# Kernel optimization log

Hardware: AMD Instinct MI355X
Metric: run time of the kernel (lower is better)

The kernel has to match this reference:

```python
import jax, jax.numpy as jnp
import numpy as np

B, N, OBS, ACT, H = 262144, 3, 30, 5, 64
IN = OBS + ACT  # 35
NEG_SLOPE_ATT = 0.2   # PyG GATConv default
NEG_SLOPE_MLP = 0.01
LN_EPS = 1e-5


def setup_inputs() -> dict:
    key = jax.random.key(0)
    ks = jax.random.split(key, 24)
    p = lambda k, shape, s=0.1: jax.random.normal(k, shape, jnp.float32) * s
    return {
        "obs": jax.random.normal(ks[0], (B, N * OBS), jnp.float32),
        "action": jax.random.normal(ks[1], (B, N * ACT), jnp.float32),
        "adj_matrix": jax.random.randint(ks[2], (B, N, N), 0, 2, jnp.int32),
        # GAT layer 1 (in=35 -> out=64, 1 head)
        "W1": p(ks[3], (IN, H)), "a1s": p(ks[4], (H,)), "a1d": p(ks[5], (H,)), "b1": jnp.zeros((H,), jnp.float32),
        # GAT layer 2 (in=64 -> out=64, 1 head)
        "W2": p(ks[6], (H, H)), "a2s": p(ks[7], (H,)), "a2d": p(ks[8], (H,)), "b2": jnp.zeros((H,), jnp.float32),
        # output_net: Linear(192,256)+LN, Linear(256,128)+LN, Linear(128,1)
        "Wo1": p(ks[9], (N * H, 256)), "bo1": jnp.zeros((256,), jnp.float32),
        "g1": jnp.ones((256,), jnp.float32), "be1": jnp.zeros((256,), jnp.float32),
        "Wo2": p(ks[10], (256, 128)), "bo2": jnp.zeros((128,), jnp.float32),
        "g2": jnp.ones((128,), jnp.float32), "be2": jnp.zeros((128,), jnp.float32),
        "Wo3": p(ks[11], (128, 1)), "bo3": jnp.zeros((1,), jnp.float32),
    }


def _gat(x, W, a_s, a_d, b, count):
    # x: [B,N,Din], count[b,i,j] = multiplicity of edge j->i (adj^T + self loop)
    z = jnp.einsum('bnd,de->bne', x, W)                      # [B,N,H]
    s_src = jnp.einsum('bnd,d->bn', z, a_s)                  # score contrib of source j
    s_dst = jnp.einsum('bnd,d->bn', z, a_d)                  # score contrib of target i
    e = jax.nn.leaky_relu(s_src[:, None, :] + s_dst[:, :, None], NEG_SLOPE_ATT)  # e[b,i,j]
    cnt = count.astype(z.dtype)
    m = jnp.max(jnp.where(count > 0, e, -jnp.inf), axis=-1, keepdims=True)  # self-loop guarantees finite
    p = cnt * jnp.exp(e - m)                                 # multiplicity-weighted softmax numerator
    alpha = p / jnp.sum(p, axis=-1, keepdims=True)           # [B,N,N]
    return jnp.einsum('bij,bjd->bid', alpha, z) + b


def _ln(x, g, be):
    mu = jnp.mean(x, axis=-1, keepdims=True)
    v = jnp.mean(jnp.square(x - mu), axis=-1, keepdims=True)
    return (x - mu) * jax.lax.rsqrt(v + LN_EPS) * g + be


def reference(obs, action, adj_matrix, W1, a1s, a1d, b1, W2, a2s, a2d, b2,
              Wo1, bo1, g1, be1, Wo2, bo2, g2, be2, Wo3, bo3):
    Bsz = obs.shape[0]
    x = jnp.concatenate([obs.reshape(Bsz, N, OBS), action.reshape(Bsz, N, ACT)], axis=-1)  # [B,N,35]
    # edge multiplicity: adj[b,s,t] means edge s->t; plus one self-loop per node
    count = jnp.swapaxes(adj_matrix, 1, 2) + jnp.eye(N, dtype=adj_matrix.dtype)  # count[b,i,j]
    h = jax.nn.elu(_gat(x, W1, a1s, a1d, b1, count))
    h = _gat(h, W2, a2s, a2d, b2, count)
    h = h.reshape(Bsz, N * H)
    h = jax.nn.leaky_relu(_ln(h @ Wo1 + bo1, g1, be1), NEG_SLOPE_MLP)
    h = jax.nn.leaky_relu(_ln(h @ Wo2 + bo2, g2, be2), NEG_SLOPE_MLP)
    return h @ Wo3 + bo3  # [B,1]
```

## Files before the change

kernel.cpp:

```cpp
#include <hip/hip_runtime.h>
#include <hip/hip_bf16.h>
#include <stdint.h>

#define B_TOT 262144

typedef __attribute__((ext_vector_type(8))) short bf8;
typedef __attribute__((ext_vector_type(16))) float f32x16;

__device__ __forceinline__ float bf2f(uint32_t u)   { return __uint_as_float(u << 16); }
__device__ __forceinline__ float bfhi2f(uint32_t u) { return __uint_as_float(u & 0xffff0000u); }
__device__ __forceinline__ uint32_t f2bf(float x) {
  uint32_t u = __float_as_uint(x);
  return (u + 0x7fffu + ((u >> 16) & 1u)) >> 16;
}
__device__ __forceinline__ uint32_t pkbf(float lo, float hi) {
  union { __hip_bfloat162 b; uint32_t u; } c;
  c.b = __float22bfloat162_rn(make_float2(lo, hi));
  return c.u;
}
__device__ __forceinline__ bf8 mkfrag(uint32_t w0, uint32_t w1, uint32_t w2, uint32_t w3) {
  union { uint32_t u[4]; bf8 v; } c;
  c.u[0] = w0; c.u[1] = w1; c.u[2] = w2; c.u[3] = w3;
  return c.v;
}
__device__ __forceinline__ bf8 u4bf8(uint4 v) {
  union { uint4 u; bf8 b; } c; c.u = v; return c.b;
}
__device__ __forceinline__ int swz(int c, int q) { return c * 16 + (q ^ (c & 15)); }

__global__ __launch_bounds__(256) void prep_kernel(
    const int* __restrict__ adj,
    const float* __restrict__ W1, const float* __restrict__ a1s, const float* __restrict__ a1d,
    const float* __restrict__ W2, const float* __restrict__ a2s, const float* __restrict__ a2d,
    const float* __restrict__ Wo1, const float* __restrict__ Wo2,
    uint32_t* __restrict__ cntp, uint16_t* __restrict__ W1F, uint16_t* __restrict__ W2F,
    uint16_t* __restrict__ Wo1F, uint16_t* __restrict__ Wo2F, float* __restrict__ wvec)
{
  const int gid = blockIdx.x * 256 + threadIdx.x;
  if (gid < B_TOT) {
    uint32_t cpv = 0;
    const int* ap = adj + (size_t)gid * 9;
    #pragma unroll
    for (int i = 0; i < 3; ++i)
      #pragma unroll
      for (int j = 0; j < 3; ++j) {
        uint32_t c = (uint32_t)ap[j * 3 + i] + (i == j ? 1u : 0u);
        cpv |= c << (2 * (3 * i + j));
      }
    cntp[gid] = cpv;
  }
  const int e = gid & 7, li = (gid >> 3) & 63;
  const int kfrag = 8 * (e >> 2) + 4 * (li >> 5) + (e & 3);
  if (gid < 3072) {
    const int f = gid >> 9, t = f & 1, ks = f >> 1;
    const int k = ks * 16 + kfrag, row = t * 32 + (li & 31);
    W1F[gid] = (uint16_t)f2bf(k < 35 ? W1[k * 64 + row] : 0.f);
  }
  if (gid < 4096) {
    const int f = gid >> 9, t = f & 1, ks = f >> 1;
    const int k = ks * 16 + kfrag, row = t * 32 + (li & 31);
    W2F[gid] = (uint16_t)f2bf(W2[k * 64 + row]);
  }
  if (gid < 49152) {
    const int rr = gid >> 9, t = rr & 7, ks = rr >> 3;
    const int k = ks * 16 + kfrag, col = t * 32 + (li & 31);
    Wo1F[gid] = (uint16_t)f2bf(Wo1[k * 256 + col]);
  }
  if (gid < 32768) {
    const int rr = gid >> 9, t = rr & 3, ks = rr >> 2;
    const int k = ks * 16 + kfrag, col = t * 32 + (li & 31);
    Wo2F[gid] = (uint16_t)f2bf(Wo2[k * 128 + col]);
  }
  if (gid < 224) {
    if (gid < 48) {
      float s = 0.f; if (gid < 35) for (int d = 0; d < 64; ++d) s += W1[gid * 64 + d] * a1s[d];
      wvec[gid] = s;
    } else if (gid < 96) {
      const int k = gid - 48; float s = 0.f;
      if (k < 35) for (int d = 0; d < 64; ++d) s += W1[k * 64 + d] * a1d[d];
      wvec[64 + k] = s;
    } else if (gid < 160) {
      const int k = gid - 96; float s = 0.f;
      for (int d = 0; d < 64; ++d) s += W2[k * 64 + d] * a2s[d];
      wvec[128 + k] = s;
    } else {
      const int k = gid - 160; float s = 0.f;
      for (int d = 0; d < 64; ++d) s += W2[k * 64 + d] * a2d[d];
      wvec[192 + k] = s;
    }
  }
}

__device__ __forceinline__ void att_alpha(const float (&ss)[3], const float (&sd)[3],
                                          uint32_t cp, float (&al)[3][3])
{
  #pragma unroll
  for (int i = 0; i < 3; ++i) {
    float ev[3]; float mx = -1e30f;
    #pragma unroll
    for (int j = 0; j < 3; ++j) {
      float s = ss[j] + sd[i];
      s = fmaxf(s, 0.2f * s);
      ev[j] = s;
      int c = (cp >> (2 * (3 * i + j))) & 3;
      mx = fmaxf(mx, c ? s : -1e30f);
    }
    float sum = 0.f;
    #pragma unroll
    for (int j = 0; j < 3; ++j) {
      int c = (cp >> (2 * (3 * i + j))) & 3;
      float p = (float)c * __expf(ev[j] - mx);
      al[i][j] = p; sum += p;
    }
    float inv = 1.0f / sum;
    #pragma unroll
    for (int j = 0; j < 3; ++j) al[i][j] *= inv;
  }
}

__device__ __forceinline__ void attention1(const f32x16 (&az)[3][2],
    const float (&ss)[3], const float (&sd)[3], uint32_t cp, int hi,
    const float* __restrict__ bvec, const float* __restrict__ nxs, const float* __restrict__ nxd,
    uint32_t (&Ph)[3][16], float (&ss2)[3], float (&sd2)[3])
{
  float al[3][3];
  att_alpha(ss, sd, cp, al);
  #pragma unroll
  for (int t = 0; t < 2; ++t) {
    float bv[16], nsv[16], ndv[16];
    #pragma unroll
    for (int rq = 0; rq < 4; ++rq) {
      float4 b4 = *reinterpret_cast<const float4*>(bvec + t * 32 + rq * 8 + hi * 4);
      float4 s4 = *reinterpret_cast<const float4*>(nxs + t * 32 + rq * 8 + hi * 4);
      float4 d4 = *reinterpret_cast<const float4*>(nxd + t * 32 + rq * 8 + hi * 4);
      bv[4 * rq + 0] = b4.x; bv[4 * rq + 1] = b4.y; bv[4 * rq + 2] = b4.z; bv[4 * rq + 3] = b4.w;
      nsv[4 * rq + 0] = s4.x; nsv[4 * rq + 1] = s4.y; nsv[4 * rq + 2] = s4.z; nsv[4 * rq + 3] = s4.w;
      ndv[4 * rq + 0] = d4.x; ndv[4 * rq + 1] = d4.y; ndv[4 * rq + 2] = d4.z; ndv[4 * rq + 3] = d4.w;
    }
    #pragma unroll
    for (int i = 0; i < 3; ++i) {
      float hv[16];
      #pragma unroll
      for (int r = 0; r < 16; ++r) {
        float v = bv[r];
        v = fmaf(al[i][0], az[0][t][r], v);
        v = fmaf(al[i][1], az[1][t][r], v);
        v = fmaf(al[i][2], az[2][t][r], v);
        v = v > 0.f ? v : (__expf(v) - 1.f);
        ss2[i] = fmaf(v, nsv[r], ss2[i]); sd2[i] = fmaf(v, ndv[r], sd2[i]);
        hv[r] = v;
      }
      #pragma unroll
      for (int p = 0; p < 8; ++p) Ph[i][t * 8 + p] = pkbf(hv[2 * p], hv[2 * p + 1]);
    }
  }
}

__device__ __forceinline__ void attention2(const f32x16 (&az)[3][2],
    const float (&ss)[3], const float (&sd)[3], uint32_t cp, int hi,
    const float* __restrict__ bvec, uint4* __restrict__ b4p, int c_own)
{
  float al[3][3];
  att_alpha(ss, sd, cp, al);
  #pragma unroll
  for (int t = 0; t < 2; ++t) {
    float bv[16];
    #pragma unroll
    for (int rq = 0; rq < 4; ++rq) {
      float4 b4 = *reinterpret_cast<const float4*>(bvec + t * 32 + rq * 8 + hi * 4);
      bv[4 * rq + 0] = b4.x; bv[4 * rq + 1] = b4.y; bv[4 * rq + 2] = b4.z; bv[4 * rq + 3] = b4.w;
    }
    #pragma unroll
    for (int i = 0; i < 3; ++i) {
      float hv[16];
      #pragma unroll
      for (int r = 0; r < 16; ++r) {
        float v = bv[r];
        v = fmaf(al[i][0], az[0][t][r], v);
        v = fmaf(al[i][1], az[1][t][r], v);
        v = fmaf(al[i][2], az[2][t][r], v);
        hv[r] = v;
      }
      uint32_t w0 = pkbf(hv[0], hv[1]),  w1 = pkbf(hv[2], hv[3]);
      uint32_t w2 = pkbf(hv[4], hv[5]),  w3 = pkbf(hv[6], hv[7]);
      uint32_t w4 = pkbf(hv[8], hv[9]),  w5 = pkbf(hv[10], hv[11]);
      uint32_t w6 = pkbf(hv[12], hv[13]), w7 = pkbf(hv[14], hv[15]);
      b4p[swz(c_own, i * 4 + t * 2 + 0)] = make_uint4(w0, w1, w2, w3);
      b4p[swz(c_own, i * 4 + t * 2 + 1)] = make_uint4(w4, w5, w6, w7);
    }
  }
}

__global__ __launch_bounds__(256, 2) void fused_kernel(
    const float* __restrict__ obs, const float* __restrict__ act,
    const uint32_t* __restrict__ cntp,
    const uint16_t* __restrict__ W1F, const uint16_t* __restrict__ W2F,
    const float* __restrict__ b1, const float* __restrict__ b2,
    const uint16_t* __restrict__ Wo1F, const float* __restrict__ bo1,
    const float* __restrict__ g1, const float* __restrict__ be1,
    const uint16_t* __restrict__ Wo2F, const float* __restrict__ bo2,
    const float* __restrict__ g2, const float* __restrict__ be2,
    const float* __restrict__ Wo3, const float* __restrict__ bo3,
    const float* __restrict__ wvec, float* __restrict__ out)
{
  __shared__ __align__(16) uint32_t buf[16384];
  __shared__ float part[1536];
  uint4* b4p = (uint4*)buf;
  const uint4* b4c = (const uint4*)buf;
  const int tid = threadIdx.x;
  const int l = tid & 63, hi = l >> 5, col = l & 31;
  const int w = tid >> 6;
  const int eb = w * 32 + col;
  const int e = blockIdx.x * 128 + eb;
  const uint32_t cp = cntp[e];
  const float* obs_e = obs + (size_t)e * 90;
  const float* act_e = act + (size_t)e * 15;

  f32x16 az[3][2];
  #pragma unroll
  for (int n = 0; n < 3; ++n)
    #pragma unroll
    for (int t = 0; t < 2; ++t)
      #pragma unroll
      for (int r = 0; r < 16; ++r) az[n][t][r] = 0.f;
  float ss1[3] = {0, 0, 0}, sd1[3] = {0, 0, 0};

  #pragma unroll
  for (int ks = 0; ks < 3; ++ks) {
    bf8 xh[3];
    #pragma unroll
    for (int n = 0; n < 3; ++n) {
      const float* on = obs_e + n * 30;
      float xv[8];
      #pragma unroll
      for (int r2 = 0; r2 < 2; ++r2) {
        if (ks == 2 && r2 == 1) { xv[4] = xv[5] = xv[6] = xv[7] = 0.f; continue; }
        const int kb = ks * 16 + r2 * 8 + hi * 4;
        #pragma unroll
        for (int j = 0; j < 4; ++j) {
          const int k = kb + j;
          float v = 0.f;
          if (k < 30) v = on[k];
          else if (k < 35) v = act_e[n * 5 + (k - 30)];
          xv[r2 * 4 + j] = v;
        }
        float4 s4 = *reinterpret_cast<const float4*>(wvec + kb);
        float4 d4 = *reinterpret_cast<const float4*>(wvec + 64 + kb);
        ss1[n] = fmaf(xv[r2 * 4 + 0], s4.x, ss1[n]); sd1[n] = fmaf(xv[r2 * 4 + 0], d4.x, sd1[n]);
        ss1[n] = fmaf(xv[r2 * 4 + 1], s4.y, ss1[n]); sd1[n] = fmaf(xv[r2 * 4 + 1], d4.y, sd1[n]);
        ss1[n] = fmaf(xv[r2 * 4 + 2], s4.z, ss1[n]); sd1[n] = fmaf(xv[r2 * 4 + 2], d4.z, sd1[n]);
        ss1[n] = fmaf(xv[r2 * 4 + 3], s4.w, ss1[n]); sd1[n] = fmaf(xv[r2 * 4 + 3], d4.w, sd1[n]);
      }
      xh[n] = mkfrag(pkbf(xv[0], xv[1]), pkbf(xv[2], xv[3]),
                     pkbf(xv[4], xv[5]), pkbf(xv[6], xv[7]));
    }
    #pragma unroll
    for (int t = 0; t < 2; ++t) {
      bf8 a = *reinterpret_cast<const bf8*>(W1F + (size_t)(ks * 2 + t) * 512 + l * 8);
      #pragma unroll
      for (int n = 0; n < 3; ++n)
        az[n][t] = __builtin_amdgcn_mfma_f32_32x32x16_bf16(a, xh[n], az[n][t], 0, 0, 0);
    }
  }
  #pragma unroll
  for (int n = 0; n < 3; ++n) {
    ss1[n] += __shfl_xor(ss1[n], 32);
    sd1[n] += __shfl_xor(sd1[n], 32);
  }

  uint32_t Ph1[3][16];
  float ss2[3] = {0, 0, 0}, sd2[3] = {0, 0, 0};
  attention1(az, ss1, sd1, cp, hi, b1, wvec + 128, wvec + 192, Ph1, ss2, sd2);
  #pragma unroll
  for (int n = 0; n < 3; ++n) {
    ss2[n] += __shfl_xor(ss2[n], 32);
    sd2[n] += __shfl_xor(sd2[n], 32);
  }

  f32x16 a2[3][2];
  #pragma unroll
  for (int n = 0; n < 3; ++n)
    #pragma unroll
    for (int t = 0; t < 2; ++t)
      #pragma unroll
      for (int r = 0; r < 16; ++r) a2[n][t][r] = 0.f;
  #pragma unroll
  for (int ks = 0; ks < 4; ++ks) {
    #pragma unroll
    for (int t = 0; t < 2; ++t) {
      bf8 a = *reinterpret_cast<const bf8*>(W2F + (size_t)(ks * 2 + t) * 512 + l * 8);
      #pragma unroll
      for (int n = 0; n < 3; ++n) {
        bf8 br_ = mkfrag(Ph1[n][4 * ks], Ph1[n][4 * ks + 1], Ph1[n][4 * ks + 2], Ph1[n][4 * ks + 3]);
        a2[n][t] = __builtin_amdgcn_mfma_f32_32x32x16_bf16(a, br_, a2[n][t], 0, 0, 0);
      }
    }
  }

  attention2(a2, ss2, sd2, cp, hi, b2, b4p, hi * 128 + eb);
  __syncthreads();

  const int fb1 = w * 64;
  f32x16 acc[2][4];
  #pragma unroll
  for (int t = 0; t < 2; ++t)
    #pragma unroll
    for (int rq = 0; rq < 4; ++rq) {
      float4 b4 = *reinterpret_cast<const float4*>(bo1 + fb1 + t * 32 + rq * 8 + hi * 4);
      #pragma unroll
      for (int eg = 0; eg < 4; ++eg) {
        acc[t][eg][4 * rq + 0] = b4.x; acc[t][eg][4 * rq + 1] = b4.y;
        acc[t][eg][4 * rq + 2] = b4.z; acc[t][eg][4 * rq + 3] = b4.w;
      }
    }
  #pragma unroll
  for (int ks = 0; ks < 12; ++ks) {
    bf8 bfr[4];
    #pragma unroll
    for (int eg = 0; eg < 4; ++eg)
      bfr[eg] = u4bf8(b4c[swz(hi * 128 + eg * 32 + col, ks)]);
    #pragma unroll
    for (int t = 0; t < 2; ++t) {
      bf8 a = *reinterpret_cast<const bf8*>(Wo1F + (size_t)(ks * 8 + w * 2 + t) * 512 + l * 8);
      #pragma unroll
      for (int eg = 0; eg < 4; ++eg)
        acc[t][eg] = __builtin_amdgcn_mfma_f32_32x32x16_bf16(a, bfr[eg], acc[t][eg], 0, 0, 0);
    }
  }
  {
    float psm[4], psq[4];
    #pragma unroll
    for (int eg = 0; eg < 4; ++eg) { psm[eg] = 0.f; psq[eg] = 0.f; }
    #pragma unroll
    for (int t = 0; t < 2; ++t)
      #pragma unroll
      for (int eg = 0; eg < 4; ++eg)
        #pragma unroll
        for (int r = 0; r < 16; ++r) {
          const float v = acc[t][eg][r]; psm[eg] += v; psq[eg] = fmaf(v, v, psq[eg]);
        }
    #pragma unroll
    for (int eg = 0; eg < 4; ++eg) {
      psm[eg] += __shfl_xor(psm[eg], 32);
      psq[eg] += __shfl_xor(psq[eg], 32);
      if (hi == 0) {
        part[w * 128 + eg * 32 + col] = psm[eg];
        part[512 + w * 128 + eg * 32 + col] = psq[eg];
      }
    }
  }
  __syncthreads();
  float mu1[4], rr1[4];
  #pragma unroll
  for (int eg = 0; eg < 4; ++eg) {
    const int ei = eg * 32 + col;
    float s = part[ei] + part[128 + ei] + part[256 + ei] + part[384 + ei];
    float q = part[512 + ei] + part[640 + ei] + part[768 + ei] + part[896 + ei];
    mu1[eg] = s * (1.f / 256.f);
    rr1[eg] = rsqrtf(q * (1.f / 256.f) - mu1[eg] * mu1[eg] + 1e-5f);
  }
  #pragma unroll
  for (int t = 0; t < 2; ++t) {
    float gv[16], bv[16];
    #pragma unroll
    for (int rq = 0; rq < 4; ++rq) {
      float4 gg = *reinterpret_cast<const float4*>(g1 + fb1 + t * 32 + rq * 8 + hi * 4);
      float4 bb = *reinterpret_cast<const float4*>(be1 + fb1 + t * 32 + rq * 8 + hi * 4);
      gv[4 * rq + 0] = gg.x; gv[4 * rq + 1] = gg.y; gv[4 * rq + 2] = gg.z; gv[4 * rq + 3] = gg.w;
      bv[4 * rq + 0] = bb.x; bv[4 * rq + 1] = bb.y; bv[4 * rq + 2] = bb.z; bv[4 * rq + 3] = bb.w;
    }
    #pragma unroll
    for (int eg = 0; eg < 4; ++eg) {
      uint32_t wd[8];
      #pragma unroll
      for (int p = 0; p < 8; ++p) {
        float va = (acc[t][eg][2 * p]     - mu1[eg]) * rr1[eg] * gv[2 * p]     + bv[2 * p];
        float vb = (acc[t][eg][2 * p + 1] - mu1[eg]) * rr1[eg] * gv[2 * p + 1] + bv[2 * p + 1];
        va = fmaxf(va, 0.01f * va);
        vb = fmaxf(vb, 0.01f * vb);
        wd[p] = pkbf(va, vb);
      }
      const int c = hi * 128 + eg * 32 + col;
      b4p[swz(c, w * 4 + t * 2 + 0)] = make_uint4(wd[0], wd[1], wd[2], wd[3]);
      b4p[swz(c, w * 4 + t * 2 + 1)] = make_uint4(wd[4], wd[5], wd[6], wd[7]);
    }
  }
  __syncthreads();

  const int fb2 = w * 32;
  f32x16 acc2[4];
  #pragma unroll
  for (int rq = 0; rq < 4; ++rq) {
    float4 b4 = *reinterpret_cast<const float4*>(bo2 + fb2 + rq * 8 + hi * 4);
    #pragma unroll
    for (int eg = 0; eg < 4; ++eg) {
      acc2[eg][4 * rq + 0] = b4.x; acc2[eg][4 * rq + 1] = b4.y;
      acc2[eg][4 * rq + 2] = b4.z; acc2[eg][4 * rq + 3] = b4.w;
    }
  }
  #pragma unroll
  for (int ks = 0; ks < 16; ++ks) {
    bf8 bfr[4];
    #pragma unroll
    for (int eg = 0; eg < 4; ++eg)
      bfr[eg] = u4bf8(b4c[swz(hi * 128 + eg * 32 + col, ks)]);
    bf8 a = *reinterpret_cast<const bf8*>(Wo2F + (size_t)(ks * 4 + w) * 512 + l * 8);
    #pragma unroll
    for (int eg = 0; eg < 4; ++eg)
      acc2[eg] = __builtin_amdgcn_mfma_f32_32x32x16_bf16(a, bfr[eg], acc2[eg], 0, 0, 0);
  }
  {
    float psm[4], psq[4];
    #pragma unroll
    for (int eg = 0; eg < 4; ++eg) { psm[eg] = 0.f; psq[eg] = 0.f; }
    #pragma unroll
    for (int eg = 0; eg < 4; ++eg)
      #pragma unroll
      for (int r = 0; r < 16; ++r) {
        const float v = acc2[eg][r]; psm[eg] += v; psq[eg] = fmaf(v, v, psq[eg]);
      }
    #pragma unroll
    for (int eg = 0; eg < 4; ++eg) {
      psm[eg] += __shfl_xor(psm[eg], 32);
      psq[eg] += __shfl_xor(psq[eg], 32);
      if (hi == 0) {
        part[w * 128 + eg * 32 + col] = psm[eg];
        part[512 + w * 128 + eg * 32 + col] = psq[eg];
      }
    }
  }
  __syncthreads();
  {
    float dot[4];
    #pragma unroll
    for (int eg = 0; eg < 4; ++eg) {
      const int ei = eg * 32 + col;
      float s = part[ei] + part[128 + ei] + part[256 + ei] + part[384 + ei];
      float q = part[512 + ei] + part[640 + ei] + part[768 + ei] + part[896 + ei];
      const float mu = s * (1.f / 128.f);
      const float rr = rsqrtf(q * (1.f / 128.f) - mu * mu + 1e-5f);
      float d = 0.f;
      #pragma unroll
      for (int rq = 0; rq < 4; ++rq) {
        float4 gg = *reinterpret_cast<const float4*>(g2 + fb2 + rq * 8 + hi * 4);
        float4 bb = *reinterpret_cast<const float4*>(be2 + fb2 + rq * 8 + hi * 4);
        float4 ww = *reinterpret_cast<const float4*>(Wo3 + fb2 + rq * 8 + hi * 4);
        float v;
        v = (acc2[eg][4 * rq + 0] - mu) * rr * gg.x + bb.x; d = fmaf(fmaxf(v, 0.01f * v), ww.x, d);
        v = (acc2[eg][4 * rq + 1] - mu) * rr * gg.y + bb.y; d = fmaf(fmaxf(v, 0.01f * v), ww.y, d);
        v = (acc2[eg][4 * rq + 2] - mu) * rr * gg.z + bb.z; d = fmaf(fmaxf(v, 0.01f * v), ww.z, d);
        v = (acc2[eg][4 * rq + 3] - mu) * rr * gg.w + bb.w; d = fmaf(fmaxf(v, 0.01f * v), ww.w, d);
      }
      dot[eg] = d;
    }
    #pragma unroll
    for (int eg = 0; eg < 4; ++eg) {
      dot[eg] += __shfl_xor(dot[eg], 32);
      if (hi == 0) part[1024 + w * 128 + eg * 32 + col] = dot[eg];
    }
  }
  __syncthreads();
  if (tid < 128) {
    out[blockIdx.x * 128 + tid] = part[1024 + tid] + part[1152 + tid] +
                                  part[1280 + tid] + part[1408 + tid] + bo3[0];
  }
}

extern "C" void kernel_launch(void* const* d_in, const int* in_sizes, int n_in,
                              void* d_out, int out_size, void* d_ws, size_t ws_size,
                              hipStream_t stream) {
  const float* obs  = (const float*)d_in[0];
  const float* actn = (const float*)d_in[1];
  const int*   adj  = (const int*)d_in[2];
  const float* W1   = (const float*)d_in[3];
  const float* a1s  = (const float*)d_in[4];
  const float* a1d  = (const float*)d_in[5];
  const float* b1   = (const float*)d_in[6];
  const float* W2   = (const float*)d_in[7];
  const float* a2s  = (const float*)d_in[8];
  const float* a2d  = (const float*)d_in[9];
  const float* b2   = (const float*)d_in[10];
  const float* Wo1  = (const float*)d_in[11];
  const float* bo1  = (const float*)d_in[12];
  const float* g1   = (const float*)d_in[13];
  const float* be1  = (const float*)d_in[14];
  const float* Wo2  = (const float*)d_in[15];
  const float* bo2  = (const float*)d_in[16];
  const float* g2   = (const float*)d_in[17];
  const float* be2  = (const float*)d_in[18];
  const float* Wo3  = (const float*)d_in[19];
  const float* bo3  = (const float*)d_in[20];

  char* ws = (char*)d_ws;
  uint32_t* cntp = (uint32_t*)ws;
  uint16_t* W1F  = (uint16_t*)(ws + 1048576);
  uint16_t* W2F  = (uint16_t*)(ws + 1048576 + 8192);
  uint16_t* Wo1F = (uint16_t*)(ws + 1048576 + 16384);
  uint16_t* Wo2F = (uint16_t*)(ws + 1048576 + 114688);
  float*    wvec = (float*)(ws + 1048576 + 180224);
  float* outp = (float*)d_out;

  prep_kernel<<<1024, 256, 0, stream>>>(adj, W1, a1s, a1d, W2, a2s, a2d, Wo1, Wo2,
                                        cntp, W1F, W2F, Wo1F, Wo2F, wvec);
  fused_kernel<<<2048, 256, 0, stream>>>(obs, actn, cntp, W1F, W2F, b1, b2,
                                         Wo1F, bo1, g1, be1, Wo2F, bo2, g2, be2,
                                         Wo3, bo3, wvec, outp);
}
```

Measured before the change: 114.0 us.

## Halve elements per block and split GAT feature halves across waves

```diff
diff --git a/kernel.cpp b/kernel.cpp
--- a/kernel.cpp
+++ b/kernel.cpp
@@ -7,8 +7,6 @@
 typedef __attribute__((ext_vector_type(8))) short bf8;
 typedef __attribute__((ext_vector_type(16))) float f32x16;
 
-__device__ __forceinline__ float bf2f(uint32_t u)   { return __uint_as_float(u << 16); }
-__device__ __forceinline__ float bfhi2f(uint32_t u) { return __uint_as_float(u & 0xffff0000u); }
 __device__ __forceinline__ uint32_t f2bf(float x) {
   uint32_t u = __float_as_uint(x);
   return (u + 0x7fffu + ((u >> 16) & 1u)) >> 16;
@@ -26,7 +24,6 @@
 __device__ __forceinline__ bf8 u4bf8(uint4 v) {
   union { uint4 u; bf8 b; } c; c.u = v; return c.b;
 }
-__device__ __forceinline__ int swz(int c, int q) { return c * 16 + (q ^ (c & 15)); }
 
 __global__ __launch_bounds__(256) void prep_kernel(
     const int* __restrict__ adj,
@@ -118,80 +115,7 @@
   }
 }
 
-__device__ __forceinline__ void attention1(const f32x16 (&az)[3][2],
-    const float (&ss)[3], const float (&sd)[3], uint32_t cp, int hi,
-    const float* __restrict__ bvec, const float* __restrict__ nxs, const float* __restrict__ nxd,
-    uint32_t (&Ph)[3][16], float (&ss2)[3], float (&sd2)[3])
-{
-  float al[3][3];
-  att_alpha(ss, sd, cp, al);
-  #pragma unroll
-  for (int t = 0; t < 2; ++t) {
-    float bv[16], nsv[16], ndv[16];
-    #pragma unroll
-    for (int rq = 0; rq < 4; ++rq) {
-      float4 b4 = *reinterpret_cast<const float4*>(bvec + t * 32 + rq * 8 + hi * 4);
-      float4 s4 = *reinterpret_cast<const float4*>(nxs + t * 32 + rq * 8 + hi * 4);
-      float4 d4 = *reinterpret_cast<const float4*>(nxd + t * 32 + rq * 8 + hi * 4);
-      bv[4 * rq + 0] = b4.x; bv[4 * rq + 1] = b4.y; bv[4 * rq + 2] = b4.z; bv[4 * rq + 3] = b4.w;
-      nsv[4 * rq + 0] = s4.x; nsv[4 * rq + 1] = s4.y; nsv[4 * rq + 2] = s4.z; nsv[4 * rq + 3] = s4.w;
-      ndv[4 * rq + 0] = d4.x; ndv[4 * rq + 1] = d4.y; ndv[4 * rq + 2] = d4.z; ndv[4 * rq + 3] = d4.w;
-    }
-    #pragma unroll
-    for (int i = 0; i < 3; ++i) {
-      float hv[16];
-      #pragma unroll
-      for (int r = 0; r < 16; ++r) {
-        float v = bv[r];
-        v = fmaf(al[i][0], az[0][t][r], v);
-        v = fmaf(al[i][1], az[1][t][r], v);
-        v = fmaf(al[i][2], az[2][t][r], v);
-        v = v > 0.f ? v : (__expf(v) - 1.f);
-        ss2[i] = fmaf(v, nsv[r], ss2[i]); sd2[i] = fmaf(v, ndv[r], sd2[i]);
-        hv[r] = v;
-      }
-      #pragma unroll
-      for (int p = 0; p < 8; ++p) Ph[i][t * 8 + p] = pkbf(hv[2 * p], hv[2 * p + 1]);
-    }
-  }
-}
-
-__device__ __forceinline__ void attention2(const f32x16 (&az)[3][2],
-    const float (&ss)[3], const float (&sd)[3], uint32_t cp, int hi,
-    const float* __restrict__ bvec, uint4* __restrict__ b4p, int c_own)
-{
-  float al[3][3];
-  att_alpha(ss, sd, cp, al);
-  #pragma unroll
-  for (int t = 0; t < 2; ++t) {
-    float bv[16];
-    #pragma unroll
-    for (int rq = 0; rq < 4; ++rq) {
-      float4 b4 = *reinterpret_cast<const float4*>(bvec + t * 32 + rq * 8 + hi * 4);
-      bv[4 * rq + 0] = b4.x; bv[4 * rq + 1] = b4.y; bv[4 * rq + 2] = b4.z; bv[4 * rq + 3] = b4.w;
-    }
-    #pragma unroll
-    for (int i = 0; i < 3; ++i) {
-      float hv[16];
-      #pragma unroll
-      for (int r = 0; r < 16; ++r) {
-        float v = bv[r];
-        v = fmaf(al[i][0], az[0][t][r], v);
-        v = fmaf(al[i][1], az[1][t][r], v);
-        v = fmaf(al[i][2], az[2][t][r], v);
-        hv[r] = v;
-      }
-      uint32_t w0 = pkbf(hv[0], hv[1]),  w1 = pkbf(hv[2], hv[3]);
-      uint32_t w2 = pkbf(hv[4], hv[5]),  w3 = pkbf(hv[6], hv[7]);
-      uint32_t w4 = pkbf(hv[8], hv[9]),  w5 = pkbf(hv[10], hv[11]);
-      uint32_t w6 = pkbf(hv[12], hv[13]), w7 = pkbf(hv[14], hv[15]);
-      b4p[swz(c_own, i * 4 + t * 2 + 0)] = make_uint4(w0, w1, w2, w3);
-      b4p[swz(c_own, i * 4 + t * 2 + 1)] = make_uint4(w4, w5, w6, w7);
-    }
-  }
-}
-
-__global__ __launch_bounds__(256, 2) void fused_kernel(
+__global__ __launch_bounds__(256, 3) void fused_kernel(
     const float* __restrict__ obs, const float* __restrict__ act,
     const uint32_t* __restrict__ cntp,
     const uint16_t* __restrict__ W1F, const uint16_t* __restrict__ W2F,
@@ -203,26 +127,23 @@
     const float* __restrict__ Wo3, const float* __restrict__ bo3,
     const float* __restrict__ wvec, float* __restrict__ out)
 {
-  __shared__ __align__(16) uint32_t buf[16384];
-  __shared__ float part[1536];
-  uint4* b4p = (uint4*)buf;
-  const uint4* b4c = (const uint4*)buf;
+  __shared__ __align__(16) uint4 buf4[3072];
+  __shared__ float part[1024];
   const int tid = threadIdx.x;
   const int l = tid & 63, hi = l >> 5, col = l & 31;
-  const int w = tid >> 6;
-  const int eb = w * 32 + col;
-  const int e = blockIdx.x * 128 + eb;
+  const int w = tid >> 6, ft = w & 1;
+  const int ebk = (w >> 1) * 32 + col;
+  const int e = blockIdx.x * 64 + ebk;
   const uint32_t cp = cntp[e];
   const float* obs_e = obs + (size_t)e * 90;
   const float* act_e = act + (size_t)e * 15;
-
-  f32x16 az[3][2];
+  const int cH0 = hi * 64 + ebk;
+
+  f32x16 az[3];
   #pragma unroll
   for (int n = 0; n < 3; ++n)
     #pragma unroll
-    for (int t = 0; t < 2; ++t)
-      #pragma unroll
-      for (int r = 0; r < 16; ++r) az[n][t][r] = 0.f;
+    for (int r = 0; r < 16; ++r) az[n][r] = 0.f;
   float ss1[3] = {0, 0, 0}, sd1[3] = {0, 0, 0};
 
   #pragma unroll
@@ -254,13 +175,10 @@
       xh[n] = mkfrag(pkbf(xv[0], xv[1]), pkbf(xv[2], xv[3]),
                      pkbf(xv[4], xv[5]), pkbf(xv[6], xv[7]));
     }
-    #pragma unroll
-    for (int t = 0; t < 2; ++t) {
-      bf8 a = *reinterpret_cast<const bf8*>(W1F + (size_t)(ks * 2 + t) * 512 + l * 8);
-      #pragma unroll
-      for (int n = 0; n < 3; ++n)
-        az[n][t] = __builtin_amdgcn_mfma_f32_32x32x16_bf16(a, xh[n], az[n][t], 0, 0, 0);
-    }
+    bf8 a = *reinterpret_cast<const bf8*>(W1F + (size_t)(ks * 2 + ft) * 512 + l * 8);
+    #pragma unroll
+    for (int n = 0; n < 3; ++n)
+      az[n] = __builtin_amdgcn_mfma_f32_32x32x16_bf16(a, xh[n], az[n], 0, 0, 0);
   }
   #pragma unroll
   for (int n = 0; n < 3; ++n) {
@@ -268,94 +186,162 @@
     sd1[n] += __shfl_xor(sd1[n], 32);
   }
 
-  uint32_t Ph1[3][16];
-  float ss2[3] = {0, 0, 0}, sd2[3] = {0, 0, 0};
-  attention1(az, ss1, sd1, cp, hi, b1, wvec + 128, wvec + 192, Ph1, ss2, sd2);
-  #pragma unroll
-  for (int n = 0; n < 3; ++n) {
-    ss2[n] += __shfl_xor(ss2[n], 32);
-    sd2[n] += __shfl_xor(sd2[n], 32);
-  }
-
-  f32x16 a2[3][2];
+  {
+    float al[3][3];
+    att_alpha(ss1, sd1, cp, al);
+    float bv[16], nsv[16], ndv[16];
+    #pragma unroll
+    for (int rq = 0; rq < 4; ++rq) {
+      float4 b4 = *reinterpret_cast<const float4*>(b1 + ft * 32 + rq * 8 + hi * 4);
+      float4 s4 = *reinterpret_cast<const float4*>(wvec + 128 + ft * 32 + rq * 8 + hi * 4);
+      float4 d4 = *reinterpret_cast<const float4*>(wvec + 192 + ft * 32 + rq * 8 + hi * 4);
+      bv[4 * rq + 0] = b4.x; bv[4 * rq + 1] = b4.y; bv[4 * rq + 2] = b4.z; bv[4 * rq + 3] = b4.w;
+      nsv[4 * rq + 0] = s4.x; nsv[4 * rq + 1] = s4.y; nsv[4 * rq + 2] = s4.z; nsv[4 * rq + 3] = s4.w;
+      ndv[4 * rq + 0] = d4.x; ndv[4 * rq + 1] = d4.y; ndv[4 * rq + 2] = d4.z; ndv[4 * rq + 3] = d4.w;
+    }
+    float s2p[3] = {0, 0, 0}, d2p[3] = {0, 0, 0};
+    #pragma unroll
+    for (int i = 0; i < 3; ++i) {
+      float hv[16];
+      #pragma unroll
+      for (int r = 0; r < 16; ++r) {
+        float v = bv[r];
+        v = fmaf(al[i][0], az[0][r], v);
+        v = fmaf(al[i][1], az[1][r], v);
+        v = fmaf(al[i][2], az[2][r], v);
+        v = v > 0.f ? v : (__expf(v) - 1.f);
+        s2p[i] = fmaf(v, nsv[r], s2p[i]);
+        d2p[i] = fmaf(v, ndv[r], d2p[i]);
+        hv[r] = v;
+      }
+      const int c = i * 128 + cH0;
+      buf4[c * 8 + ((ft * 2 + 0) ^ (c & 7))] =
+          make_uint4(pkbf(hv[0], hv[1]), pkbf(hv[2], hv[3]), pkbf(hv[4], hv[5]), pkbf(hv[6], hv[7]));
+      buf4[c * 8 + ((ft * 2 + 1) ^ (c & 7))] =
+          make_uint4(pkbf(hv[8], hv[9]), pkbf(hv[10], hv[11]), pkbf(hv[12], hv[13]), pkbf(hv[14], hv[15]));
+    }
+    #pragma unroll
+    for (int i = 0; i < 3; ++i) {
+      s2p[i] += __shfl_xor(s2p[i], 32);
+      d2p[i] += __shfl_xor(d2p[i], 32);
+      if (hi == 0) {
+        part[ft * 192 + i * 64 + ebk] = s2p[i];
+        part[384 + ft * 192 + i * 64 + ebk] = d2p[i];
+      }
+    }
+  }
+  __syncthreads();
+
+  float ss2[3], sd2[3];
+  #pragma unroll
+  for (int i = 0; i < 3; ++i) {
+    ss2[i] = part[i * 64 + ebk] + part[192 + i * 64 + ebk];
+    sd2[i] = part[384 + i * 64 + ebk] + part[576 + i * 64 + ebk];
+  }
+
+  f32x16 a2[3];
   #pragma unroll
   for (int n = 0; n < 3; ++n)
     #pragma unroll
-    for (int t = 0; t < 2; ++t)
-      #pragma unroll
-      for (int r = 0; r < 16; ++r) a2[n][t][r] = 0.f;
+    for (int r = 0; r < 16; ++r) a2[n][r] = 0.f;
   #pragma unroll
   for (int ks = 0; ks < 4; ++ks) {
-    #pragma unroll
-    for (int t = 0; t < 2; ++t) {
-      bf8 a = *reinterpret_cast<const bf8*>(W2F + (size_t)(ks * 2 + t) * 512 + l * 8);
-      #pragma unroll
-      for (int n = 0; n < 3; ++n) {
-        bf8 br_ = mkfrag(Ph1[n][4 * ks], Ph1[n][4 * ks + 1], Ph1[n][4 * ks + 2], Ph1[n][4 * ks + 3]);
-        a2[n][t] = __builtin_amdgcn_mfma_f32_32x32x16_bf16(a, br_, a2[n][t], 0, 0, 0);
-      }
-    }
-  }
-
-  attention2(a2, ss2, sd2, cp, hi, b2, b4p, hi * 128 + eb);
+    bf8 aW = *reinterpret_cast<const bf8*>(W2F + (size_t)(ks * 2 + ft) * 512 + l * 8);
+    #pragma unroll
+    for (int n = 0; n < 3; ++n) {
+      const int c = n * 128 + cH0;
+      bf8 b = u4bf8(buf4[c * 8 + (ks ^ (c & 7))]);
+      a2[n] = __builtin_amdgcn_mfma_f32_32x32x16_bf16(aW, b, a2[n], 0, 0, 0);
+    }
+  }
+  __syncthreads();
+
+  {
+    float al[3][3];
+    att_alpha(ss2, sd2, cp, al);
+    float bv[16];
+    #pragma unroll
+    for (int rq = 0; rq < 4; ++rq) {
+      float4 b4 = *reinterpret_cast<const float4*>(b2 + ft * 32 + rq * 8 + hi * 4);
+      bv[4 * rq + 0] = b4.x; bv[4 * rq + 1] = b4.y; bv[4 * rq + 2] = b4.z; bv[4 * rq + 3] = b4.w;
+    }
+    #pragma unroll
+    for (int i = 0; i < 3; ++i) {
+      float hv[16];
+      #pragma unroll
+      for (int r = 0; r < 16; ++r) {
+        float v = bv[r];
+        v = fmaf(al[i][0], a2[0][r], v);
+        v = fmaf(al[i][1], a2[1][r], v);
+        v = fmaf(al[i][2], a2[2][r], v);
+        hv[r] = v;
+      }
+      const int c = i * 128 + cH0;
+      buf4[c * 8 + ((ft * 2 + 0) ^ (c & 7))] =
+          make_uint4(pkbf(hv[0], hv[1]), pkbf(hv[2], hv[3]), pkbf(hv[4], hv[5]), pkbf(hv[6], hv[7]));
+      buf4[c * 8 + ((ft * 2 + 1) ^ (c & 7))] =
+          make_uint4(pkbf(hv[8], hv[9]), pkbf(hv[10], hv[11]), pkbf(hv[12], hv[13]), pkbf(hv[14], hv[15]));
+    }
+  }
   __syncthreads();
 
   const int fb1 = w * 64;
-  f32x16 acc[2][4];
+  f32x16 acc[2][2];
   #pragma unroll
   for (int t = 0; t < 2; ++t)
     #pragma unroll
     for (int rq = 0; rq < 4; ++rq) {
       float4 b4 = *reinterpret_cast<const float4*>(bo1 + fb1 + t * 32 + rq * 8 + hi * 4);
       #pragma unroll
-      for (int eg = 0; eg < 4; ++eg) {
+      for (int eg = 0; eg < 2; ++eg) {
         acc[t][eg][4 * rq + 0] = b4.x; acc[t][eg][4 * rq + 1] = b4.y;
         acc[t][eg][4 * rq + 2] = b4.z; acc[t][eg][4 * rq + 3] = b4.w;
       }
     }
   #pragma unroll
   for (int ks = 0; ks < 12; ++ks) {
-    bf8 bfr[4];
-    #pragma unroll
-    for (int eg = 0; eg < 4; ++eg)
-      bfr[eg] = u4bf8(b4c[swz(hi * 128 + eg * 32 + col, ks)]);
+    const int n = ks >> 2, q = ks & 3;
+    bf8 bfr[2];
+    #pragma unroll
+    for (int eg = 0; eg < 2; ++eg) {
+      const int c = n * 128 + hi * 64 + eg * 32 + col;
+      bfr[eg] = u4bf8(buf4[c * 8 + (q ^ (c & 7))]);
+    }
     #pragma unroll
     for (int t = 0; t < 2; ++t) {
       bf8 a = *reinterpret_cast<const bf8*>(Wo1F + (size_t)(ks * 8 + w * 2 + t) * 512 + l * 8);
       #pragma unroll
-      for (int eg = 0; eg < 4; ++eg)
+      for (int eg = 0; eg < 2; ++eg)
         acc[t][eg] = __builtin_amdgcn_mfma_f32_32x32x16_bf16(a, bfr[eg], acc[t][eg], 0, 0, 0);
     }
   }
   {
-    float psm[4], psq[4];
-    #pragma unroll
-    for (int eg = 0; eg < 4; ++eg) { psm[eg] = 0.f; psq[eg] = 0.f; }
+    float psm[2] = {0, 0}, psq[2] = {0, 0};
     #pragma unroll
     for (int t = 0; t < 2; ++t)
       #pragma unroll
-      for (int eg = 0; eg < 4; ++eg)
+      for (int eg = 0; eg < 2; ++eg)
         #pragma unroll
         for (int r = 0; r < 16; ++r) {
           const float v = acc[t][eg][r]; psm[eg] += v; psq[eg] = fmaf(v, v, psq[eg]);
         }
     #pragma unroll
-    for (int eg = 0; eg < 4; ++eg) {
+    for (int eg = 0; eg < 2; ++eg) {
       psm[eg] += __shfl_xor(psm[eg], 32);
       psq[eg] += __shfl_xor(psq[eg], 32);
       if (hi == 0) {
-        part[w * 128 + eg * 32 + col] = psm[eg];
-        part[512 + w * 128 + eg * 32 + col] = psq[eg];
-      }
-    }
-  }
-  __syncthreads();
-  float mu1[4], rr1[4];
-  #pragma unroll
-  for (int eg = 0; eg < 4; ++eg) {
+        part[w * 64 + eg * 32 + col] = psm[eg];
+        part[256 + w * 64 + eg * 32 + col] = psq[eg];
+      }
+    }
+  }
+  __syncthreads();
+  float mu1[2], rr1[2];
+  #pragma unroll
+  for (int eg = 0; eg < 2; ++eg) {
     const int ei = eg * 32 + col;
-    float s = part[ei] + part[128 + ei] + part[256 + ei] + part[384 + ei];
-    float q = part[512 + ei] + part[640 + ei] + part[768 + ei] + part[896 + ei];
+    float s = part[ei] + part[64 + ei] + part[128 + ei] + part[192 + ei];
+    float q = part[256 + ei] + part[320 + ei] + part[384 + ei] + part[448 + ei];
     mu1[eg] = s * (1.f / 256.f);
     rr1[eg] = rsqrtf(q * (1.f / 256.f) - mu1[eg] * mu1[eg] + 1e-5f);
   }
@@ -370,7 +356,7 @@
       bv[4 * rq + 0] = bb.x; bv[4 * rq + 1] = bb.y; bv[4 * rq + 2] = bb.z; bv[4 * rq + 3] = bb.w;
     }
     #pragma unroll
-    for (int eg = 0; eg < 4; ++eg) {
+    for (int eg = 0; eg < 2; ++eg) {
       uint32_t wd[8];
       #pragma unroll
       for (int p = 0; p < 8; ++p) {
@@ -380,63 +366,64 @@
         vb = fmaxf(vb, 0.01f * vb);
         wd[p] = pkbf(va, vb);
       }
-      const int c = hi * 128 + eg * 32 + col;
-      b4p[swz(c, w * 4 + t * 2 + 0)] = make_uint4(wd[0], wd[1], wd[2], wd[3]);
-      b4p[swz(c, w * 4 + t * 2 + 1)] = make_uint4(wd[4], wd[5], wd[6], wd[7]);
+      const int cy = hi * 64 + eg * 32 + col;
+      const int g0 = w * 4 + t * 2;
+      buf4[cy * 16 + (g0 ^ (cy & 15))]       = make_uint4(wd[0], wd[1], wd[2], wd[3]);
+      buf4[cy * 16 + ((g0 + 1) ^ (cy & 15))] = make_uint4(wd[4], wd[5], wd[6], wd[7]);
     }
   }
   __syncthreads();
 
   const int fb2 = w * 32;
-  f32x16 acc2[4];
+  f32x16 acc2[2];
   #pragma unroll
   for (int rq = 0; rq < 4; ++rq) {
     float4 b4 = *reinterpret_cast<const float4*>(bo2 + fb2 + rq * 8 + hi * 4);
     #pragma unroll
-    for (int eg = 0; eg < 4; ++eg) {
+    for (int eg = 0; eg < 2; ++eg) {
       acc2[eg][4 * rq + 0] = b4.x; acc2[eg][4 * rq + 1] = b4.y;
       acc2[eg][4 * rq + 2] = b4.z; acc2[eg][4 * rq + 3] = b4.w;
     }
   }
   #pragma unroll
   for (int ks = 0; ks < 16; ++ks) {
-    bf8 bfr[4];
-    #pragma unroll
-    for (int eg = 0; eg < 4; ++eg)
-      bfr[eg] = u4bf8(b4c[swz(hi * 128 + eg * 32 + col, ks)]);
+    bf8 bfr[2];
+    #pragma unroll
+    for (int eg = 0; eg < 2; ++eg) {
+      const int cy = hi * 64 + eg * 32 + col;
+      bfr[eg] = u4bf8(buf4[cy * 16 + (ks ^ (cy & 15))]);
+    }
     bf8 a = *reinterpret_cast<const bf8*>(Wo2F + (size_t)(ks * 4 + w) * 512 + l * 8);
     #pragma unroll
-    for (int eg = 0; eg < 4; ++eg)
+    for (int eg = 0; eg < 2; ++eg)
       acc2[eg] = __builtin_amdgcn_mfma_f32_32x32x16_bf16(a, bfr[eg], acc2[eg], 0, 0, 0);
   }
   {
-    float psm[4], psq[4];
-    #pragma unroll
-    for (int eg = 0; eg < 4; ++eg) { psm[eg] = 0.f; psq[eg] = 0.f; }
-    #pragma unroll
-    for (int eg = 0; eg < 4; ++eg)
+    float psm[2] = {0, 0}, psq[2] = {0, 0};
+    #pragma unroll
+    for (int eg = 0; eg < 2; ++eg)
       #pragma unroll
       for (int r = 0; r < 16; ++r) {
         const float v = acc2[eg][r]; psm[eg] += v; psq[eg] = fmaf(v, v, psq[eg]);
       }
     #pragma unroll
-    for (int eg = 0; eg < 4; ++eg) {
+    for (int eg = 0; eg < 2; ++eg) {
       psm[eg] += __shfl_xor(psm[eg], 32);
       psq[eg] += __shfl_xor(psq[eg], 32);
       if (hi == 0) {
-        part[w * 128 + eg * 32 + col] = psm[eg];
-        part[512 + w * 128 + eg * 32 + col] = psq[eg];
+        part[w * 64 + eg * 32 + col] = psm[eg];
+        part[256 + w * 64 + eg * 32 + col] = psq[eg];
       }
     }
   }
   __syncthreads();
   {
-    float dot[4];
-    #pragma unroll
-    for (int eg = 0; eg < 4; ++eg) {
+    float dot[2];
+    #pragma unroll
+    for (int eg = 0; eg < 2; ++eg) {
       const int ei = eg * 32 + col;
-      float s = part[ei] + part[128 + ei] + part[256 + ei] + part[384 + ei];
-      float q = part[512 + ei] + part[640 + ei] + part[768 + ei] + part[896 + ei];
+      float s = part[ei] + part[64 + ei] + part[128 + ei] + part[192 + ei];
+      float q = part[256 + ei] + part[320 + ei] + part[384 + ei] + part[448 + ei];
       const float mu = s * (1.f / 128.f);
       const float rr = rsqrtf(q * (1.f / 128.f) - mu * mu + 1e-5f);
       float d = 0.f;
@@ -454,15 +441,15 @@
       dot[eg] = d;
     }
     #pragma unroll
-    for (int eg = 0; eg < 4; ++eg) {
+    for (int eg = 0; eg < 2; ++eg) {
       dot[eg] += __shfl_xor(dot[eg], 32);
-      if (hi == 0) part[1024 + w * 128 + eg * 32 + col] = dot[eg];
-    }
-  }
-  __syncthreads();
-  if (tid < 128) {
-    out[blockIdx.x * 128 + tid] = part[1024 + tid] + part[1152 + tid] +
-                                  part[1280 + tid] + part[1408 + tid] + bo3[0];
+      if (hi == 0) part[512 + w * 64 + eg * 32 + col] = dot[eg];
+    }
+  }
+  __syncthreads();
+  if (tid < 64) {
+    out[blockIdx.x * 64 + tid] = part[512 + tid] + part[576 + tid] +
+                                 part[640 + tid] + part[704 + tid] + bo3[0];
   }
 }
 
@@ -502,7 +489,7 @@
 
   prep_kernel<<<1024, 256, 0, stream>>>(adj, W1, a1s, a1d, W2, a2s, a2d, Wo1, Wo2,
                                         cntp, W1F, W2F, Wo1F, Wo2F, wvec);
-  fused_kernel<<<2048, 256, 0, stream>>>(obs, actn, cntp, W1F, W2F, b1, b2,
+  fused_kernel<<<4096, 256, 0, stream>>>(obs, actn, cntp, W1F, W2F, b1, b2,
                                          Wo1F, bo1, g1, be1, Wo2F, bo2, g2, be2,
                                          Wo3, bo3, wvec, outp);
 }
```

New measurement: 162.6 us. +42.7%, slower.

## Fold GAT attention score projections into extra MFMA tiles

Applied to the files above, without the earlier changes.

```diff
diff --git a/kernel.cpp b/kernel.cpp
--- a/kernel.cpp
+++ b/kernel.cpp
@@ -7,8 +7,6 @@
 typedef __attribute__((ext_vector_type(8))) short bf8;
 typedef __attribute__((ext_vector_type(16))) float f32x16;
 
-__device__ __forceinline__ float bf2f(uint32_t u)   { return __uint_as_float(u << 16); }
-__device__ __forceinline__ float bfhi2f(uint32_t u) { return __uint_as_float(u & 0xffff0000u); }
 __device__ __forceinline__ uint32_t f2bf(float x) {
   uint32_t u = __float_as_uint(x);
   return (u + 0x7fffu + ((u >> 16) & 1u)) >> 16;
@@ -34,7 +32,7 @@
     const float* __restrict__ W2, const float* __restrict__ a2s, const float* __restrict__ a2d,
     const float* __restrict__ Wo1, const float* __restrict__ Wo2,
     uint32_t* __restrict__ cntp, uint16_t* __restrict__ W1F, uint16_t* __restrict__ W2F,
-    uint16_t* __restrict__ Wo1F, uint16_t* __restrict__ Wo2F, float* __restrict__ wvec)
+    uint16_t* __restrict__ Wo1F, uint16_t* __restrict__ Wo2F)
 {
   const int gid = blockIdx.x * 256 + threadIdx.x;
   if (gid < B_TOT) {
@@ -51,15 +49,25 @@
   }
   const int e = gid & 7, li = (gid >> 3) & 63;
   const int kfrag = 8 * (e >> 2) + 4 * (li >> 5) + (e & 3);
-  if (gid < 3072) {
-    const int f = gid >> 9, t = f & 1, ks = f >> 1;
+  if (gid < 4608) {
+    const int f = gid >> 9, t = f % 3, ks = f / 3;
     const int k = ks * 16 + kfrag, row = t * 32 + (li & 31);
-    W1F[gid] = (uint16_t)f2bf(k < 35 ? W1[k * 64 + row] : 0.f);
-  }
-  if (gid < 4096) {
-    const int f = gid >> 9, t = f & 1, ks = f >> 1;
+    float v = 0.f;
+    if (k < 35) {
+      if (row < 64) v = W1[k * 64 + row];
+      else if (row == 64) { float s = 0; for (int d = 0; d < 64; ++d) s += W1[k * 64 + d] * a1s[d]; v = s; }
+      else if (row == 65) { float s = 0; for (int d = 0; d < 64; ++d) s += W1[k * 64 + d] * a1d[d]; v = s; }
+    }
+    W1F[gid] = (uint16_t)f2bf(v);
+  }
+  if (gid < 6144) {
+    const int f = gid >> 9, t = f % 3, ks = f / 3;
     const int k = ks * 16 + kfrag, row = t * 32 + (li & 31);
-    W2F[gid] = (uint16_t)f2bf(W2[k * 64 + row]);
+    float v = 0.f;
+    if (row < 64) v = W2[k * 64 + row];
+    else if (row == 64) { float s = 0; for (int d = 0; d < 64; ++d) s += W2[k * 64 + d] * a2s[d]; v = s; }
+    else if (row == 65) { float s = 0; for (int d = 0; d < 64; ++d) s += W2[k * 64 + d] * a2d[d]; v = s; }
+    W2F[gid] = (uint16_t)f2bf(v);
   }
   if (gid < 49152) {
     const int rr = gid >> 9, t = rr & 7, ks = rr >> 3;
@@ -70,24 +78,6 @@
     const int rr = gid >> 9, t = rr & 3, ks = rr >> 2;
     const int k = ks * 16 + kfrag, col = t * 32 + (li & 31);
     Wo2F[gid] = (uint16_t)f2bf(Wo2[k * 128 + col]);
-  }
-  if (gid < 224) {
-    if (gid < 48) {
-      float s = 0.f; if (gid < 35) for (int d = 0; d < 64; ++d) s += W1[gid * 64 + d] * a1s[d];
-      wvec[gid] = s;
-    } else if (gid < 96) {
-      const int k = gid - 48; float s = 0.f;
-      if (k < 35) for (int d = 0; d < 64; ++d) s += W1[k * 64 + d] * a1d[d];
-      wvec[64 + k] = s;
-    } else if (gid < 160) {
-      const int k = gid - 96; float s = 0.f;
-      for (int d = 0; d < 64; ++d) s += W2[k * 64 + d] * a2s[d];
-      wvec[128 + k] = s;
-    } else {
-      const int k = gid - 160; float s = 0.f;
-      for (int d = 0; d < 64; ++d) s += W2[k * 64 + d] * a2d[d];
-      wvec[192 + k] = s;
-    }
   }
 }
 
@@ -120,22 +110,17 @@
 
 __device__ __forceinline__ void attention1(const f32x16 (&az)[3][2],
     const float (&ss)[3], const float (&sd)[3], uint32_t cp, int hi,
-    const float* __restrict__ bvec, const float* __restrict__ nxs, const float* __restrict__ nxd,
-    uint32_t (&Ph)[3][16], float (&ss2)[3], float (&sd2)[3])
+    const float* __restrict__ bvec, uint32_t (&Ph)[3][16])
 {
   float al[3][3];
   att_alpha(ss, sd, cp, al);
   #pragma unroll
   for (int t = 0; t < 2; ++t) {
-    float bv[16], nsv[16], ndv[16];
+    float bv[16];
     #pragma unroll
     for (int rq = 0; rq < 4; ++rq) {
       float4 b4 = *reinterpret_cast<const float4*>(bvec + t * 32 + rq * 8 + hi * 4);
-      float4 s4 = *reinterpret_cast<const float4*>(nxs + t * 32 + rq * 8 + hi * 4);
-      float4 d4 = *reinterpret_cast<const float4*>(nxd + t * 32 + rq * 8 + hi * 4);
       bv[4 * rq + 0] = b4.x; bv[4 * rq + 1] = b4.y; bv[4 * rq + 2] = b4.z; bv[4 * rq + 3] = b4.w;
-      nsv[4 * rq + 0] = s4.x; nsv[4 * rq + 1] = s4.y; nsv[4 * rq + 2] = s4.z; nsv[4 * rq + 3] = s4.w;
-      ndv[4 * rq + 0] = d4.x; ndv[4 * rq + 1] = d4.y; ndv[4 * rq + 2] = d4.z; ndv[4 * rq + 3] = d4.w;
     }
     #pragma unroll
     for (int i = 0; i < 3; ++i) {
@@ -147,7 +132,6 @@
         v = fmaf(al[i][1], az[1][t][r], v);
         v = fmaf(al[i][2], az[2][t][r], v);
         v = v > 0.f ? v : (__expf(v) - 1.f);
-        ss2[i] = fmaf(v, nsv[r], ss2[i]); sd2[i] = fmaf(v, ndv[r], sd2[i]);
         hv[r] = v;
       }
       #pragma unroll
@@ -201,7 +185,7 @@
     const uint16_t* __restrict__ Wo2F, const float* __restrict__ bo2,
     const float* __restrict__ g2, const float* __restrict__ be2,
     const float* __restrict__ Wo3, const float* __restrict__ bo3,
-    const float* __restrict__ wvec, float* __restrict__ out)
+    float* __restrict__ out)
 {
   __shared__ __align__(16) uint32_t buf[16384];
   __shared__ float part[1536];
@@ -216,14 +200,16 @@
   const float* obs_e = obs + (size_t)e * 90;
   const float* act_e = act + (size_t)e * 15;
 
-  f32x16 az[3][2];
-  #pragma unroll
-  for (int n = 0; n < 3; ++n)
+  f32x16 az[3][2], azs[3];
+  #pragma unroll
+  for (int n = 0; n < 3; ++n) {
     #pragma unroll
     for (int t = 0; t < 2; ++t)
       #pragma unroll
       for (int r = 0; r < 16; ++r) az[n][t][r] = 0.f;
-  float ss1[3] = {0, 0, 0}, sd1[3] = {0, 0, 0};
+    #pragma unroll
+    for (int r = 0; r < 16; ++r) azs[n][r] = 0.f;
+  }
 
   #pragma unroll
   for (int ks = 0; ks < 3; ++ks) {
@@ -244,57 +230,69 @@
           else if (k < 35) v = act_e[n * 5 + (k - 30)];
           xv[r2 * 4 + j] = v;
         }
-        float4 s4 = *reinterpret_cast<const float4*>(wvec + kb);
-        float4 d4 = *reinterpret_cast<const float4*>(wvec + 64 + kb);
-        ss1[n] = fmaf(xv[r2 * 4 + 0], s4.x, ss1[n]); sd1[n] = fmaf(xv[r2 * 4 + 0], d4.x, sd1[n]);
-        ss1[n] = fmaf(xv[r2 * 4 + 1], s4.y, ss1[n]); sd1[n] = fmaf(xv[r2 * 4 + 1], d4.y, sd1[n]);
-        ss1[n] = fmaf(xv[r2 * 4 + 2], s4.z, ss1[n]); sd1[n] = fmaf(xv[r2 * 4 + 2], d4.z, sd1[n]);
-        ss1[n] = fmaf(xv[r2 * 4 + 3], s4.w, ss1[n]); sd1[n] = fmaf(xv[r2 * 4 + 3], d4.w, sd1[n]);
       }
       xh[n] = mkfrag(pkbf(xv[0], xv[1]), pkbf(xv[2], xv[3]),
                      pkbf(xv[4], xv[5]), pkbf(xv[6], xv[7]));
     }
     #pragma unroll
     for (int t = 0; t < 2; ++t) {
-      bf8 a = *reinterpret_cast<const bf8*>(W1F + (size_t)(ks * 2 + t) * 512 + l * 8);
+      bf8 a = *reinterpret_cast<const bf8*>(W1F + (size_t)(ks * 3 + t) * 512 + l * 8);
       #pragma unroll
       for (int n = 0; n < 3; ++n)
         az[n][t] = __builtin_amdgcn_mfma_f32_32x32x16_bf16(a, xh[n], az[n][t], 0, 0, 0);
     }
-  }
+    {
+      bf8 as_ = *reinterpret_cast<const bf8*>(W1F + (size_t)(ks * 3 + 2) * 512 + l * 8);
+      #pragma unroll
+      for (int n = 0; n < 3; ++n)
+        azs[n] = __builtin_amdgcn_mfma_f32_32x32x16_bf16(as_, xh[n], azs[n], 0, 0, 0);
+    }
+  }
+  float ss1[3], sd1[3];
   #pragma unroll
   for (int n = 0; n < 3; ++n) {
-    ss1[n] += __shfl_xor(ss1[n], 32);
-    sd1[n] += __shfl_xor(sd1[n], 32);
+    ss1[n] = __shfl(azs[n][0], col);
+    sd1[n] = __shfl(azs[n][1], col);
   }
 
   uint32_t Ph1[3][16];
-  float ss2[3] = {0, 0, 0}, sd2[3] = {0, 0, 0};
-  attention1(az, ss1, sd1, cp, hi, b1, wvec + 128, wvec + 192, Ph1, ss2, sd2);
+  attention1(az, ss1, sd1, cp, hi, b1, Ph1);
+
+  f32x16 a2[3][2], a2s_[3];
   #pragma unroll
   for (int n = 0; n < 3; ++n) {
-    ss2[n] += __shfl_xor(ss2[n], 32);
-    sd2[n] += __shfl_xor(sd2[n], 32);
-  }
-
-  f32x16 a2[3][2];
-  #pragma unroll
-  for (int n = 0; n < 3; ++n)
     #pragma unroll
     for (int t = 0; t < 2; ++t)
       #pragma unroll
       for (int r = 0; r < 16; ++r) a2[n][t][r] = 0.f;
+    #pragma unroll
+    for (int r = 0; r < 16; ++r) a2s_[n][r] = 0.f;
+  }
   #pragma unroll
   for (int ks = 0; ks < 4; ++ks) {
+    bf8 br[3];
+    #pragma unroll
+    for (int n = 0; n < 3; ++n)
+      br[n] = mkfrag(Ph1[n][4 * ks], Ph1[n][4 * ks + 1], Ph1[n][4 * ks + 2], Ph1[n][4 * ks + 3]);
     #pragma unroll
     for (int t = 0; t < 2; ++t) {
-      bf8 a = *reinterpret_cast<const bf8*>(W2F + (size_t)(ks * 2 + t) * 512 + l * 8);
-      #pragma unroll
-      for (int n = 0; n < 3; ++n) {
-        bf8 br_ = mkfrag(Ph1[n][4 * ks], Ph1[n][4 * ks + 1], Ph1[n][4 * ks + 2], Ph1[n][4 * ks + 3]);
-        a2[n][t] = __builtin_amdgcn_mfma_f32_32x32x16_bf16(a, br_, a2[n][t], 0, 0, 0);
-      }
-    }
+      bf8 aW = *reinterpret_cast<const bf8*>(W2F + (size_t)(ks * 3 + t) * 512 + l * 8);
+      #pragma unroll
+      for (int n = 0; n < 3; ++n)
+        a2[n][t] = __builtin_amdgcn_mfma_f32_32x32x16_bf16(aW, br[n], a2[n][t], 0, 0, 0);
+    }
+    {
+      bf8 aS = *reinterpret_cast<const bf8*>(W2F + (size_t)(ks * 3 + 2) * 512 + l * 8);
+      #pragma unroll
+      for (int n = 0; n < 3; ++n)
+        a2s_[n] = __builtin_amdgcn_mfma_f32_32x32x16_bf16(aS, br[n], a2s_[n], 0, 0, 0);
+    }
+  }
+  float ss2[3], sd2[3];
+  #pragma unroll
+  for (int n = 0; n < 3; ++n) {
+    ss2[n] = __shfl(a2s_[n][0], col);
+    sd2[n] = __shfl(a2s_[n][1], col);
   }
 
   attention2(a2, ss2, sd2, cp, hi, b2, b4p, hi * 128 + eb);
@@ -494,15 +492,14 @@
   char* ws = (char*)d_ws;
   uint32_t* cntp = (uint32_t*)ws;
   uint16_t* W1F  = (uint16_t*)(ws + 1048576);
-  uint16_t* W2F  = (uint16_t*)(ws + 1048576 + 8192);
-  uint16_t* Wo1F = (uint16_t*)(ws + 1048576 + 16384);
-  uint16_t* Wo2F = (uint16_t*)(ws + 1048576 + 114688);
-  float*    wvec = (float*)(ws + 1048576 + 180224);
+  uint16_t* W2F  = (uint16_t*)(ws + 1048576 + 16384);
+  uint16_t* Wo1F = (uint16_t*)(ws + 1048576 + 32768);
+  uint16_t* Wo2F = (uint16_t*)(ws + 1048576 + 131072);
   float* outp = (float*)d_out;
 
   prep_kernel<<<1024, 256, 0, stream>>>(adj, W1, a1s, a1d, W2, a2s, a2d, Wo1, Wo2,
-                                        cntp, W1F, W2F, Wo1F, Wo2F, wvec);
+                                        cntp, W1F, W2F, Wo1F, Wo2F);
   fused_kernel<<<2048, 256, 0, stream>>>(obs, actn, cntp, W1F, W2F, b1, b2,
                                          Wo1F, bo1, g1, be1, Wo2F, bo2, g2, be2,
-                                         Wo3, bo3, wvec, outp);
-}
+                                         Wo3, bo3, outp);
+}
```

Measured after the change: 125.0 us. 9.7% more time.
